# Performance work log

Measured on AMD Instinct MI355X. Metric: run time of the kernel, lower is better.

The kernel has to match this reference:

```python
import jax, jax.numpy as jnp
import numpy as np

NUM_CLASSES = 32
TRI = NUM_CLASSES * (NUM_CLASSES - 1) // 2      # 496 class pairs
HID = 32 * TRI                                  # 15872 total hidden
IN = 512
B = 256
RATIO = 0.0

# pair -> (i, j) class indices, in the same enumeration order as the torch idx formula
_I_IDX, _J_IDX = np.triu_indices(NUM_CLASSES, k=1)
_I_IDX = jnp.asarray(_I_IDX)
_J_IDX = jnp.asarray(_J_IDX)


def setup_inputs() -> dict:
    key = jax.random.key(0)
    ks = jax.random.split(key, 7)
    s = 0.02  # small init so activations stay sane
    return {
        "x": jax.random.normal(ks[0], (B, IN), jnp.float32),
        "W1": jax.random.normal(ks[1], (IN, HID), jnp.float32) * s,
        "b1": jax.random.normal(ks[2], (HID,), jnp.float32) * s,
        "W2": jax.random.normal(ks[3], (HID, HID), jnp.float32) * s,
        "b2": jax.random.normal(ks[4], (HID,), jnp.float32) * s,
        "Wout": jax.random.normal(ks[5], (HID, 2 * TRI), jnp.float32) * s,
        "bout": jax.random.normal(ks[6], (2 * TRI,), jnp.float32) * s,
    }


def reference(x, W1, b1, W2, b2, Wout, bout):
    # MLP stack: fc1 + relu, fc2 + relu (num_layers=2), fc_out
    h = jax.nn.relu(x @ W1 + b1)                 # [B, HID]
    h = jax.nn.relu(h @ W2 + b2)                 # [B, HID]
    out = h @ Wout + bout                        # [B, 2*TRI]

    # vote scatter: out[:, 2p], out[:, 2p+1] are the (i, j) logits of pair p
    pair = out.reshape(B, TRI, 2)                # [B, TRI, 2]
    d = pair[..., 0] - pair[..., 1]              # [B, TRI]
    # original condition: d > ratio  OR  -d >= ratio   (always true at ratio=0)
    mask = (d > RATIO) | (-d >= RATIO)
    vi = jnp.where(mask, pair[..., 0], 0.0)      # contribution to class i
    vj = jnp.where(mask, pair[..., 1], 0.0)      # contribution to class j

    votes = jnp.zeros((B, NUM_CLASSES), jnp.float32)
    votes = votes.at[:, _I_IDX].add(vi)
    votes = votes.at[:, _J_IDX].add(vj)
    return votes
```

## Files before the change

kernel.cpp:

```cpp
#include <hip/hip_runtime.h>
#include <hip/hip_bf16.h>

using short8 = __attribute__((ext_vector_type(8))) short;
using f32x16 = __attribute__((ext_vector_type(16))) float;
using us4    = __attribute__((ext_vector_type(4))) unsigned short;

#define NHID 15872

__device__ __forceinline__ unsigned short f2bf(float f) {
  unsigned u = __builtin_bit_cast(unsigned, f);
  u += 0x7fff + ((u >> 16) & 1);
  return (unsigned short)(u >> 16);
}
__device__ __forceinline__ short f2bf_hw(float f) {
  __hip_bfloat16 h = __float2bfloat16(f);
  return __builtin_bit_cast(short, h);
}
__device__ __forceinline__ float bf2f(unsigned short h) {
  return __builtin_bit_cast(float, ((unsigned)h) << 16);
}

__device__ __forceinline__ void gload16(const void* g, void* l) {
  __builtin_amdgcn_global_load_lds(
      (const __attribute__((address_space(1))) unsigned int*)g,
      (__attribute__((address_space(3))) unsigned int*)l, 16, 0, 0);
}

__device__ __forceinline__ size_t pk_idx(int row, int col) {
  return (size_t)(col >> 4) * 4096 +
         (size_t)(row + 256 * ((col >> 3) & 1)) * 8 + (col & 7);
}

__global__ void cvt_x_pack(const float* __restrict__ x, unsigned short* __restrict__ xpk) {
  int g = blockIdx.x * 256 + threadIdx.x;
  int row = g >> 6, k0 = (g & 63) * 8;
  const float* p = x + (size_t)row * 512 + k0;
  float4 a = *reinterpret_cast<const float4*>(p);
  float4 b = *reinterpret_cast<const float4*>(p + 4);
  us4 o0, o1;
  o0[0] = f2bf(a.x); o0[1] = f2bf(a.y); o0[2] = f2bf(a.z); o0[3] = f2bf(a.w);
  o1[0] = f2bf(b.x); o1[1] = f2bf(b.y); o1[2] = f2bf(b.z); o1[3] = f2bf(b.w);
  unsigned short* d = xpk + pk_idx(row, k0);
  *reinterpret_cast<us4*>(d)     = o0;
  *reinterpret_cast<us4*>(d + 4) = o1;
}


#define WAITV(N) asm volatile("s_waitcnt vmcnt(" #N ")" ::: "memory")

#define STAGEB(BUF, T) do { _Pragma("unroll") \
  for (int j_ = 0; j_ < 4; ++j_) \
    gload16(bsrc + ((size_t)(T) * 32 + 2 * j_) * NHID, \
            &Blds[BUF][(w * 8 + 2 * j_) * 128]); \
} while (0)

#define LOADA(T) do { \
    const unsigned short* ap_ = asrc + (size_t)(T) * 8192; \
    rA[0] = *reinterpret_cast<const short8*>(ap_); \
    rA[1] = *reinterpret_cast<const short8*>(ap_ + 4096); \
    rA[2] = *reinterpret_cast<const short8*>(ap_ + 256); \
    rA[3] = *reinterpret_cast<const short8*>(ap_ + 4096 + 256); \
  } while (0)

#define COMPUTE(BC) do { \
    const float* bb_ = &Blds[BC][0]; \
    _Pragma("unroll") \
    for (int ks_ = 0; ks_ < 2; ++ks_) { \
      _Pragma("unroll") \
      for (int nb_ = 0; nb_ < 4; ++nb_) { \
        float tf_[8]; \
        _Pragma("unroll") \
        for (int jj_ = 0; jj_ < 8; ++jj_) \
          tf_[jj_] = bb_[(ks_ * 16 + hi * 8 + jj_) * 128 + nb_ * 32 + l31]; \
        short8 bfr_; \
        _Pragma("unroll") \
        for (int jj_ = 0; jj_ < 8; ++jj_) bfr_[jj_] = f2bf_hw(tf_[jj_]); \
        acc[nb_]     = __builtin_amdgcn_mfma_f32_32x32x16_bf16(rA[ks_],     bfr_, acc[nb_],     0, 0, 0); \
        acc[4 + nb_] = __builtin_amdgcn_mfma_f32_32x32x16_bf16(rA[2 + ks_], bfr_, acc[4 + nb_], 0, 0, 0); \
      } \
    } \
  } while (0)

template<int OUTMODE, bool SWZ>
__global__ __launch_bounds__(256, 3)
void gemm_v14(const unsigned short* __restrict__ Apk, int KC,
              const float* __restrict__ B, const float* __restrict__ bias,
              unsigned short* __restrict__ Cf, unsigned short* __restrict__ Cpb)
{
  __shared__ float Blds[3][32 * 128];

  int nidx, ks0;
  if (SWZ) {
    int b = blockIdx.x;
    ks0  = b & 15;
    nidx = b >> 4;
  } else {
    nidx = blockIdx.x; ks0 = blockIdx.y;
  }
  const int n0   = nidx * 128;
  const int k0   = ks0 * KC;
  const int tid  = threadIdx.x;
  const int w    = tid >> 6;
  const int lane = tid & 63;
  const int l31  = lane & 31;
  const int hi   = lane >> 5;

  f32x16 acc[8] = {};
  short8 rA[4];

  const float* bsrc = B + (size_t)(k0 + w * 8 + hi) * NHID + n0 + l31 * 4;
  const unsigned short* asrc = Apk + (size_t)(k0 >> 4) * 4096 +
                               (size_t)(w * 64 + l31 + 256 * hi) * 8;

  const int NT = KC >> 5;

  STAGEB(0, 0);
  STAGEB(1, 1);

  int bc = 0;
  for (int t = 0; t < NT; ++t) {
    WAITV(4);
    __builtin_amdgcn_sched_barrier(0);
    __builtin_amdgcn_s_barrier();
    LOADA(t);
    if (t + 2 < NT) { int sb_ = bc >= 1 ? bc - 1 : 2; STAGEB(sb_, t + 2); }
    COMPUTE(bc);
    bc = bc == 2 ? 0 : bc + 1;
  }

#pragma unroll
  for (int rb = 0; rb < 2; ++rb) {
#pragma unroll
    for (int nb = 0; nb < 4; ++nb) {
      int col = n0 + nb * 32 + l31;
      float bv = (OUTMODE != 1) ? bias[col] : 0.f;
#pragma unroll
      for (int reg = 0; reg < 16; ++reg) {
        int row = w * 64 + rb * 32 + (reg & 3) + 8 * (reg >> 2) + 4 * hi;
        float v = acc[rb * 4 + nb][reg];
        if (OUTMODE == 0) {
          v += bv; v = v > 0.f ? v : 0.f;
          Cf[pk_idx(row, col)] = f2bf(v);
        } else if (OUTMODE == 1) {
          Cpb[(size_t)ks0 * 256 * NHID + (size_t)row * NHID + col] = f2bf(v);
        } else {
          v += bv; v = v > 0.f ? v : 0.f;
          Cf[(size_t)row * NHID + col] = f2bf(v);
        }
      }
    }
  }
}

template<bool PACK>
__global__ void reduce_hb(const unsigned short* __restrict__ part,
                          const float* __restrict__ bias,
                          unsigned short* __restrict__ out, int S) {
  int g8 = blockIdx.x * 256 + threadIdx.x;
  int row = g8 / 1984;
  int c   = (g8 - row * 1984) * 8;
  size_t off = (size_t)row * NHID + c;
  float s[8] = {0.f, 0.f, 0.f, 0.f, 0.f, 0.f, 0.f, 0.f};
  for (int k = 0; k < S; ++k) {
    short8 p = *reinterpret_cast<const short8*>(part + (size_t)k * 256 * NHID + off);
#pragma unroll
    for (int j = 0; j < 8; ++j) s[j] += bf2f((unsigned short)p[j]);
  }
  short8 o;
#pragma unroll
  for (int j = 0; j < 8; ++j) {
    float v = s[j] + bias[c + j];
    v = v > 0.f ? v : 0.f;
    o[j] = (short)f2bf(v);
  }
  if (PACK) *reinterpret_cast<short8*>(out + pk_idx(row, c)) = o;
  else      *reinterpret_cast<short8*>(out + off) = o;
}

__global__ void wv_fold(const float* __restrict__ Wout, float* __restrict__ Wv) {
  int g = blockIdx.x * 256 + threadIdx.x;
  int k = g >> 5, c = g & 31;
  const float* row = Wout + (size_t)k * 992;
  float s = 0.f;
#pragma unroll
  for (int o = 0; o < 32; ++o) {
    if (o == c) continue;
    int i = c < o ? c : o;
    int j = c < o ? o : c;
    int p = 31 * i - (i * (i - 1)) / 2 + (j - i - 1);
    s += row[2 * p + (c > o ? 1 : 0)];
  }
  Wv[g] = s;
}

__global__ void votes_partial(const unsigned short* __restrict__ h2,
                              const float* __restrict__ Wv,
                              float* __restrict__ part) {
  int bm = blockIdx.x >> 5;
  int ks = blockIdx.x & 31;
  int r  = bm * 8 + (threadIdx.x >> 5);
  int c  = threadIdx.x & 31;
  const unsigned short* hrow = h2 + (size_t)r * NHID + ks * 496;
  const float* wp = Wv + (size_t)(ks * 496) * 32 + c;
  float s = 0.f;
  for (int k0 = 0; k0 < 496; k0 += 8) {
    short8 hv = *reinterpret_cast<const short8*>(hrow + k0);
#pragma unroll
    for (int j = 0; j < 8; ++j)
      s += bf2f((unsigned short)hv[j]) * wp[(size_t)(k0 + j) * 32];
  }
  part[(size_t)(ks * 256 + r) * 32 + c] = s;
}

__global__ void votes_reduce(const float* __restrict__ part,
                             const float* __restrict__ bout,
                             float* __restrict__ out) {
  int g = blockIdx.x * 256 + threadIdx.x;
  int c = g & 31;
  float s = 0.f;
#pragma unroll
  for (int ks = 0; ks < 32; ++ks) s += part[(size_t)ks * 8192 + g];
  float bv = 0.f;
#pragma unroll
  for (int o = 0; o < 32; ++o) {
    if (o == c) continue;
    int i = c < o ? c : o;
    int j = c < o ? o : c;
    int p = 31 * i - (i * (i - 1)) / 2 + (j - i - 1);
    bv += bout[2 * p + (c > o ? 1 : 0)];
  }
  out[g] = s + bv;
}

extern "C" void kernel_launch(void* const* d_in, const int* in_sizes, int n_in,
                              void* d_out, int out_size, void* d_ws, size_t ws_size,
                              hipStream_t stream) {
  const float* x    = (const float*)d_in[0];
  const float* W1   = (const float*)d_in[1];
  const float* b1   = (const float*)d_in[2];
  const float* W2   = (const float*)d_in[3];
  const float* b2   = (const float*)d_in[4];
  const float* Wout = (const float*)d_in[5];
  const float* bout = (const float*)d_in[6];
  float* out = (float*)d_out;

  char* ws = (char*)d_ws;
  unsigned short* xpk  = (unsigned short*)(ws);
  unsigned short* h1pk = (unsigned short*)(ws + 262144);
  unsigned short* h2   = (unsigned short*)(ws + 8388608);
  float*          Wv   = (float*)(ws + 16515072);
  float*          part = (float*)(ws + 18546688);
  unsigned short* pb   = (unsigned short*)(ws + 19595264);

  const size_t PARTB = (size_t)256 * NHID * 2;
  const bool split = ws_size >= 19595264ull + 16 * PARTB;

  hipLaunchKernelGGL(cvt_x_pack, dim3(64), dim3(256), 0, stream, x, xpk);
  if (split) {
    hipLaunchKernelGGL((gemm_v14<1, false>), dim3(124, 2), dim3(256), 0, stream,
                       xpk, 256, W1, (const float*)nullptr,
                       (unsigned short*)nullptr, pb);
    hipLaunchKernelGGL((reduce_hb<true>), dim3(1984), dim3(256), 0, stream,
                       pb, b1, h1pk, 2);
    hipLaunchKernelGGL((gemm_v14<1, true>), dim3(1984), dim3(256), 0, stream,
                       h1pk, 992, W2, (const float*)nullptr,
                       (unsigned short*)nullptr, pb);
    hipLaunchKernelGGL((reduce_hb<false>), dim3(1984), dim3(256), 0, stream,
                       pb, b2, h2, 16);
  } else {
    hipLaunchKernelGGL((gemm_v14<0, false>), dim3(124, 1), dim3(256), 0, stream,
                       xpk, 512, W1, b1, h1pk, (unsigned short*)nullptr);
    hipLaunchKernelGGL((gemm_v14<2, false>), dim3(124, 1), dim3(256), 0, stream,
                       h1pk, NHID, W2, b2, h2, (unsigned short*)nullptr);
  }
  hipLaunchKernelGGL(wv_fold,       dim3(1984), dim3(256), 0, stream, Wout, Wv);
  hipLaunchKernelGGL(votes_partial, dim3(1024), dim3(256), 0, stream, h2, Wv, part);
  hipLaunchKernelGGL(votes_reduce,  dim3(32),   dim3(256), 0, stream, part, bout, out);
}
```

Baseline: 449.8 us.

## Split GEMM tile across 8 waves with 2x4 warp grid and halve split-K

The GEMM kernel moves from 4 waves to 8 waves per 256x128 tile, arranged as a 4x2 (M by N) wave grid. Each wave now keeps 4 accumulators instead of 8, which lowers register pressure so more waves can be resident per CU. B staging is split across the extra waves and uses non-temporal loads, since the W2 stream is read once. The second GEMM's split-K drops from 16 to 8 slices, halving the partial-sum traffic and the reduce work, at the cost of fewer blocks and more A-fragment reloads per wave.

```diff
diff --git a/kernel.cpp b/kernel.cpp
--- a/kernel.cpp
+++ b/kernel.cpp
@@ -24,6 +24,11 @@
   __builtin_amdgcn_global_load_lds(
       (const __attribute__((address_space(1))) unsigned int*)g,
       (__attribute__((address_space(3))) unsigned int*)l, 16, 0, 0);
+}
+__device__ __forceinline__ void gload16nt(const void* g, void* l) {
+  __builtin_amdgcn_global_load_lds(
+      (const __attribute__((address_space(1))) unsigned int*)g,
+      (__attribute__((address_space(3))) unsigned int*)l, 16, 0, 2);
 }
 
 __device__ __forceinline__ size_t pk_idx(int row, int col) {
@@ -48,11 +53,10 @@
 
 #define WAITV(N) asm volatile("s_waitcnt vmcnt(" #N ")" ::: "memory")
 
-#define STAGEB(BUF, T) do { _Pragma("unroll") \
-  for (int j_ = 0; j_ < 4; ++j_) \
-    gload16(bsrc + ((size_t)(T) * 32 + 2 * j_) * NHID, \
-            &Blds[BUF][(w * 8 + 2 * j_) * 128]); \
-} while (0)
+#define STAGEB(BUF, T) do { \
+    gload16nt(bsrc + (size_t)(T) * 32 * NHID,       &Blds[BUF][(w * 4 + 0) * 128]); \
+    gload16nt(bsrc + ((size_t)(T) * 32 + 2) * NHID, &Blds[BUF][(w * 4 + 2) * 128]); \
+  } while (0)
 
 #define LOADA(T) do { \
     const unsigned short* ap_ = asrc + (size_t)(T) * 8192; \
@@ -66,24 +70,26 @@
     const float* bb_ = &Blds[BC][0]; \
     _Pragma("unroll") \
     for (int ks_ = 0; ks_ < 2; ++ks_) { \
+      short8 bfr_[2]; \
       _Pragma("unroll") \
-      for (int nb_ = 0; nb_ < 4; ++nb_) { \
+      for (int nb_ = 0; nb_ < 2; ++nb_) { \
         float tf_[8]; \
         _Pragma("unroll") \
         for (int jj_ = 0; jj_ < 8; ++jj_) \
-          tf_[jj_] = bb_[(ks_ * 16 + hi * 8 + jj_) * 128 + nb_ * 32 + l31]; \
-        short8 bfr_; \
+          tf_[jj_] = bb_[(ks_ * 16 + hi * 8 + jj_) * 128 + wn * 64 + nb_ * 32 + l31]; \
         _Pragma("unroll") \
-        for (int jj_ = 0; jj_ < 8; ++jj_) bfr_[jj_] = f2bf_hw(tf_[jj_]); \
-        acc[nb_]     = __builtin_amdgcn_mfma_f32_32x32x16_bf16(rA[ks_],     bfr_, acc[nb_],     0, 0, 0); \
-        acc[4 + nb_] = __builtin_amdgcn_mfma_f32_32x32x16_bf16(rA[2 + ks_], bfr_, acc[4 + nb_], 0, 0, 0); \
+        for (int jj_ = 0; jj_ < 8; ++jj_) bfr_[nb_][jj_] = f2bf_hw(tf_[jj_]); \
       } \
+      acc[0] = __builtin_amdgcn_mfma_f32_32x32x16_bf16(rA[ks_],     bfr_[0], acc[0], 0, 0, 0); \
+      acc[1] = __builtin_amdgcn_mfma_f32_32x32x16_bf16(rA[ks_],     bfr_[1], acc[1], 0, 0, 0); \
+      acc[2] = __builtin_amdgcn_mfma_f32_32x32x16_bf16(rA[2 + ks_], bfr_[0], acc[2], 0, 0, 0); \
+      acc[3] = __builtin_amdgcn_mfma_f32_32x32x16_bf16(rA[2 + ks_], bfr_[1], acc[3], 0, 0, 0); \
     } \
   } while (0)
 
 template<int OUTMODE, bool SWZ>
-__global__ __launch_bounds__(256, 3)
-void gemm_v14(const unsigned short* __restrict__ Apk, int KC,
+__global__ __launch_bounds__(512, 4)
+void gemm_v15(const unsigned short* __restrict__ Apk, int KC,
               const float* __restrict__ B, const float* __restrict__ bias,
               unsigned short* __restrict__ Cf, unsigned short* __restrict__ Cpb)
 {
@@ -92,8 +98,8 @@
   int nidx, ks0;
   if (SWZ) {
     int b = blockIdx.x;
-    ks0  = b & 15;
-    nidx = b >> 4;
+    ks0  = b & 7;
+    nidx = b >> 3;
   } else {
     nidx = blockIdx.x; ks0 = blockIdx.y;
   }
@@ -104,13 +110,15 @@
   const int lane = tid & 63;
   const int l31  = lane & 31;
   const int hi   = lane >> 5;
-
-  f32x16 acc[8] = {};
+  const int wm   = w >> 1;
+  const int wn   = w & 1;
+
+  f32x16 acc[4] = {};
   short8 rA[4];
 
-  const float* bsrc = B + (size_t)(k0 + w * 8 + hi) * NHID + n0 + l31 * 4;
+  const float* bsrc = B + (size_t)(k0 + w * 4 + hi) * NHID + n0 + l31 * 4;
   const unsigned short* asrc = Apk + (size_t)(k0 >> 4) * 4096 +
-                               (size_t)(w * 64 + l31 + 256 * hi) * 8;
+                               (size_t)(wm * 64 + l31 + 256 * hi) * 8;
 
   const int NT = KC >> 5;
 
@@ -119,7 +127,7 @@
 
   int bc = 0;
   for (int t = 0; t < NT; ++t) {
-    WAITV(4);
+    if (t + 1 < NT) { WAITV(2); } else { WAITV(0); }
     __builtin_amdgcn_sched_barrier(0);
     __builtin_amdgcn_s_barrier();
     LOADA(t);
@@ -131,13 +139,13 @@
 #pragma unroll
   for (int rb = 0; rb < 2; ++rb) {
 #pragma unroll
-    for (int nb = 0; nb < 4; ++nb) {
-      int col = n0 + nb * 32 + l31;
+    for (int nb = 0; nb < 2; ++nb) {
+      int col = n0 + wn * 64 + nb * 32 + l31;
       float bv = (OUTMODE != 1) ? bias[col] : 0.f;
 #pragma unroll
       for (int reg = 0; reg < 16; ++reg) {
-        int row = w * 64 + rb * 32 + (reg & 3) + 8 * (reg >> 2) + 4 * hi;
-        float v = acc[rb * 4 + nb][reg];
+        int row = wm * 64 + rb * 32 + (reg & 3) + 8 * (reg >> 2) + 4 * hi;
+        float v = acc[rb * 2 + nb][reg];
         if (OUTMODE == 0) {
           v += bv; v = v > 0.f ? v : 0.f;
           Cf[pk_idx(row, col)] = f2bf(v);
@@ -253,24 +261,24 @@
   unsigned short* pb   = (unsigned short*)(ws + 19595264);
 
   const size_t PARTB = (size_t)256 * NHID * 2;
-  const bool split = ws_size >= 19595264ull + 16 * PARTB;
+  const bool split = ws_size >= 19595264ull + 8 * PARTB;
 
   hipLaunchKernelGGL(cvt_x_pack, dim3(64), dim3(256), 0, stream, x, xpk);
   if (split) {
-    hipLaunchKernelGGL((gemm_v14<1, false>), dim3(124, 2), dim3(256), 0, stream,
+    hipLaunchKernelGGL((gemm_v15<1, false>), dim3(124, 2), dim3(512), 0, stream,
                        xpk, 256, W1, (const float*)nullptr,
                        (unsigned short*)nullptr, pb);
     hipLaunchKernelGGL((reduce_hb<true>), dim3(1984), dim3(256), 0, stream,
                        pb, b1, h1pk, 2);
-    hipLaunchKernelGGL((gemm_v14<1, true>), dim3(1984), dim3(256), 0, stream,
-                       h1pk, 992, W2, (const float*)nullptr,
+    hipLaunchKernelGGL((gemm_v15<1, true>), dim3(992), dim3(512), 0, stream,
+                       h1pk, 1984, W2, (const float*)nullptr,
                        (unsigned short*)nullptr, pb);
     hipLaunchKernelGGL((reduce_hb<false>), dim3(1984), dim3(256), 0, stream,
-                       pb, b2, h2, 16);
+                       pb, b2, h2, 8);
   } else {
-    hipLaunchKernelGGL((gemm_v14<0, false>), dim3(124, 1), dim3(256), 0, stream,
+    hipLaunchKernelGGL((gemm_v15<0, false>), dim3(124, 1), dim3(512), 0, stream,
                        xpk, 512, W1, b1, h1pk, (unsigned short*)nullptr);
-    hipLaunchKernelGGL((gemm_v14<2, false>), dim3(124, 1), dim3(256), 0, stream,
+    hipLaunchKernelGGL((gemm_v15<2, false>), dim3(124, 1), dim3(512), 0, stream,
                        h1pk, NHID, W2, b2, h2, (unsigned short*)nullptr);
   }
   hipLaunchKernelGGL(wv_fold,       dim3(1984), dim3(256), 0, stream, Wout, Wv);
```

Result: faster. 393.0 us (-12.6%).
